# Kernel optimization log

Measured on AMD Instinct MI355X. Metric: run time of the kernel, lower is better.

The kernel has to match this reference:

```python
import jax, jax.numpy as jnp
import numpy as np

T_STEPS = 10       # T_pos = T_neg = 10 hardcoded in forward
ATTN_SCALE = 0.125 # scale hardcoded in forward (not head_dim**-0.5)
V_TH = 1.0         # spikingjelly IFNode defaults: v_threshold=1.0, v_reset=0.0 (hard reset)
SG_ALPHA = 4.0     # default Sigmoid surrogate alpha

@jax.custom_vjp
def spike(v):
    return (v >= 0.0).astype(v.dtype)

def _spike_fwd(v):
    return spike(v), v

def _spike_bwd(v, g):
    sg = jax.nn.sigmoid(SG_ALPHA * v)
    return (g * SG_ALPHA * sg * (1.0 - sg),)

spike.defvjp(_spike_fwd, _spike_bwd)

def if_node_const_input(y, T=T_STEPS):
    """Multi-step IF neuron driven by the SAME input y at every step.
    charge: v += y; fire: s = H(v - 1); hard reset: v = (1 - s) * v.
    Returns spikes of shape [T, *y.shape]."""
    def step(v, _):
        v = v + y
        s = spike(v - V_TH)
        v = (1.0 - s) * v
        return v, s
    _, spikes = jax.lax.scan(step, jnp.zeros_like(y), None, length=T)
    return spikes

def setup_inputs() -> dict:
    key = jax.random.key(0)
    ks = jax.random.split(key, 6)
    N, C = 2048, 2048
    x = jax.random.normal(ks[0], (N, C), dtype=jnp.float32)
    freqs_cis = jax.random.normal(ks[1], (N, 64), dtype=jnp.float32)  # unused by forward
    w_scale = 0.02
    wq = jax.random.normal(ks[2], (C, C), dtype=jnp.float32) * w_scale
    wk = jax.random.normal(ks[3], (C, C), dtype=jnp.float32) * w_scale
    wv = jax.random.normal(ks[4], (C, C), dtype=jnp.float32) * w_scale
    wo = jax.random.normal(ks[5], (C, C), dtype=jnp.float32) * w_scale
    return {"x": x, "freqs_cis": freqs_cis, "wq": wq, "wk": wk, "wv": wv, "wo": wo}

def reference(x, freqs_cis, wq, wk, wv, wo):
    N, C = x.shape
    n_heads, head_dim = 16, 128  # C == n_heads * head_dim; n_kv_heads == n_heads so repeat_kv is a no-op
    T = T_STEPS

    x_pos = jax.nn.relu(x)
    x_neg = jax.nn.relu(-x)

    # Input is identical at every timestep, so apply the linear once, then run IF over T.
    def branch(xb):
        q = if_node_const_input(xb @ wq)  # [T, N, C] binary spikes
        k = if_node_const_input(xb @ wk)
        v = if_node_const_input(xb @ wv)
        return q, k, v

    qp, kp, vp = branch(x_pos)
    qn, kn, vn = branch(x_neg)
    xq = (qp - qn).reshape(T, N, n_heads, head_dim)
    xk = (kp - kn).reshape(T, N, n_heads, head_dim)
    xv = (vp - vn).reshape(T, N, n_heads, head_dim)

    # no-softmax attention over the HEAD axis, per token: [T,N,H,H]
    attn = jnp.einsum('tnhd,tnmd->tnhm', xq, xk) * ATTN_SCALE
    x_attn = jnp.einsum('tnhm,tnmd->tnhd', attn, xv)          # [T,N,H,Dh]
    x_attn = jnp.swapaxes(x_attn, -1, -2).reshape(T, N, C)    # transpose(-1,-2) then merge

    xo = x_attn @ wo  # [T, N, C]
    return xo.mean(axis=0)
```

## Files before the change

### kernel.cpp

```cpp
#include <hip/hip_runtime.h>
#include <hip/hip_bf16.h>


#define LIST_CAP (512u * 1024u)
#define FLAG_EPS 4e-4f

typedef __attribute__((ext_vector_type(8))) short short8;
typedef __attribute__((ext_vector_type(4))) float floatx4;

__device__ const unsigned d_LUT[16] = {0u, 0x3FFu, 0x2AAu, 0x124u, 0x88u,
                                       0x210u, 0x20u, 0x40u, 0x80u, 0x100u,
                                       0x200u, 0u, 0u, 0u, 0u, 0u};

__device__ __forceinline__ void bf16x2_rne(float a, unsigned& p1, unsigned& p2) {
  const unsigned u = __float_as_uint(a);
  const unsigned t1 = u + 0x7FFFu + ((u >> 16) & 1u);
  p1 = t1 >> 16;
  const float r = a - __uint_as_float(t1 & 0xFFFF0000u);
  const unsigned u2 = __float_as_uint(r);
  p2 = (u2 + 0x7FFFu + ((u2 >> 16) & 1u)) >> 16;
}

template <int ZERO_CNT>
__global__ __launch_bounds__(256) void wsplit(
    const float* __restrict__ W0, const float* __restrict__ W1,
    const float* __restrict__ W2, unsigned short* __restrict__ Bpk,
    int NCT, unsigned* __restrict__ cnt) {
  if (ZERO_CNT && blockIdx.x == 0 && blockIdx.y == 0 && threadIdx.x == 0)
    *cnt = 0u;
  __shared__ float Wf[32 * 132];
  const int ct = blockIdx.x, k0 = blockIdx.y * 32;
  const int c0 = ct * 128;
  const int sel = c0 >> 11;
  const float* W = (sel == 0) ? W0 : ((sel == 1) ? W1 : W2);
  const int cc0 = c0 & 2047;
  const int t = threadIdx.x;

  const int kr = t >> 3, cq = (t & 7) * 16;
#pragma unroll
  for (int u = 0; u < 4; u++) {
    const float4 v = *(const float4*)(W + (size_t)(k0 + kr) * 2048 + cc0 + cq + 4 * u);
    *(float4*)&Wf[kr * 132 + cq + 4 * u] = v;
  }
  __syncthreads();

  const int cc = t >> 1, ch0 = (t & 1) * 2;
  unsigned short* img1 = Bpk + ((size_t)(0 * NCT + ct) * 64 + blockIdx.y) * 4096;
  unsigned short* img2 = Bpk + ((size_t)(1 * NCT + ct) * 64 + blockIdx.y) * 4096;
#pragma unroll
  for (int c = ch0; c < ch0 + 2; c++) {
    unsigned q1[8], q2[8];
#pragma unroll
    for (int e = 0; e < 8; e++) bf16x2_rne(Wf[(c * 8 + e) * 132 + cc], q1[e], q2[e]);
    const int off = cc * 32 + 8 * (c ^ ((cc >> 1) & 3));
    uint4 P1, P2;
    P1.x = q1[0] | (q1[1] << 16); P1.y = q1[2] | (q1[3] << 16);
    P1.z = q1[4] | (q1[5] << 16); P1.w = q1[6] | (q1[7] << 16);
    P2.x = q2[0] | (q2[1] << 16); P2.y = q2[2] | (q2[3] << 16);
    P2.z = q2[4] | (q2[5] << 16); P2.w = q2[6] | (q2[7] << 16);
    *(uint4*)&img1[off] = P1;
    *(uint4*)&img2[off] = P2;
  }
}

template <int RELU>
__global__ __launch_bounds__(256) void asplit(
    const float* __restrict__ src, unsigned short* __restrict__ Apk, int NRT) {
  const int rt = blockIdx.x, k0i = blockIdx.y;
  const int t = threadIdx.x;
  const int r = t >> 1, half = t & 1;
  int grow = rt * 128 + r;
  float sgn = 1.f;
  if (RELU && grow >= 2048) { grow -= 2048; sgn = -1.f; }
  const float* s = src + (size_t)grow * 2048 + k0i * 32 + half * 16;
  float f[16];
#pragma unroll
  for (int u = 0; u < 4; u++) {
    const float4 v = *(const float4*)(s + 4 * u);
    f[4 * u + 0] = v.x; f[4 * u + 1] = v.y;
    f[4 * u + 2] = v.z; f[4 * u + 3] = v.w;
  }
  if (RELU) {
#pragma unroll
    for (int e = 0; e < 16; e++) f[e] = fmaxf(sgn * f[e], 0.f);
  }
  unsigned q1[16], q2[16];
#pragma unroll
  for (int e = 0; e < 16; e++) bf16x2_rne(f[e], q1[e], q2[e]);

  unsigned short* img1 = Apk + ((size_t)(0 * NRT + rt) * 64 + k0i) * 4096;
  unsigned short* img2 = Apk + ((size_t)(1 * NRT + rt) * 64 + k0i) * 4096;
#pragma unroll
  for (int cc = 0; cc < 2; cc++) {
    const int c = half * 2 + cc;
    const int off = r * 32 + 8 * (c ^ ((r >> 1) & 3));
    const int e0 = cc * 8;
    uint4 P1, P2;
    P1.x = q1[e0 + 0] | (q1[e0 + 1] << 16); P1.y = q1[e0 + 2] | (q1[e0 + 3] << 16);
    P1.z = q1[e0 + 4] | (q1[e0 + 5] << 16); P1.w = q1[e0 + 6] | (q1[e0 + 7] << 16);
    P2.x = q2[e0 + 0] | (q2[e0 + 1] << 16); P2.y = q2[e0 + 2] | (q2[e0 + 3] << 16);
    P2.z = q2[e0 + 4] | (q2[e0 + 5] << 16); P2.w = q2[e0 + 6] | (q2[e0 + 7] << 16);
    *(uint4*)&img1[off] = P1;
    *(uint4*)&img2[off] = P2;
  }
}

template <int MODE>
__global__ __launch_bounds__(256) void gemm_dma(
    const unsigned short* __restrict__ Apk, const unsigned short* __restrict__ Bpk,
    int NRT, int NCT, unsigned char* __restrict__ MaskJ,
    unsigned* __restrict__ list, unsigned* __restrict__ cnt,
    float* __restrict__ Out) {
  __shared__ unsigned short sh[2][4][4096];
  __shared__ unsigned lutS[16];

  const int tid = threadIdx.x;
  const int bx = blockIdx.x, by = blockIdx.y;
  const int lane = tid & 63, wave = tid >> 6;
  const int wr = wave >> 1, wc = wave & 1;
  const int lm = lane & 15, lg = lane >> 4;

  if (MODE == 0 && tid < 16) lutS[tid] = d_LUT[tid];

  const unsigned short* gsrc =
      (wave < 2) ? (Apk + ((size_t)(wave * NRT + by) * 64) * 4096)
                 : (Bpk + ((size_t)((wave - 2) * NCT + bx) * 64) * 4096);

  auto dma8 = [&](unsigned short* dst, const unsigned short* src) {
#pragma unroll
    for (int i = 0; i < 8; i++) {
      __builtin_amdgcn_global_load_lds(
          (const __attribute__((address_space(1))) unsigned*)(src + i * 512 + lane * 8),
          (__attribute__((address_space(3))) unsigned*)(dst + i * 512), 16, 0, 0);
    }
  };

  floatx4 acc[4][4];
#pragma unroll
  for (int i = 0; i < 4; i++)
#pragma unroll
    for (int j = 0; j < 4; j++) acc[i][j] = (floatx4){0.f, 0.f, 0.f, 0.f};

  dma8(&sh[0][wave][0], gsrc);

  for (int k0i = 0; k0i < 64; k0i++) {
    __syncthreads();
    if (k0i + 1 < 64)
      dma8(&sh[(k0i + 1) & 1][wave][0], gsrc + (size_t)(k0i + 1) * 4096);

    const unsigned short(*cur)[4096] = sh[k0i & 1];
    short8 a1[4], a2[4], b1[4], b2[4];
#pragma unroll
    for (int i = 0; i < 4; i++) {
      const int row = 64 * wr + 16 * i + lm;
      const int off = row * 32 + 8 * (lg ^ ((row >> 1) & 3));
      a1[i] = *(const short8*)&cur[0][off];
      a2[i] = *(const short8*)&cur[1][off];
    }
#pragma unroll
    for (int j = 0; j < 4; j++) {
      const int row = 64 * wc + 16 * j + lm;
      const int off = row * 32 + 8 * (lg ^ ((row >> 1) & 3));
      b1[j] = *(const short8*)&cur[2][off];
      b2[j] = *(const short8*)&cur[3][off];
    }
#pragma unroll
    for (int i = 0; i < 4; i++)
#pragma unroll
      for (int j = 0; j < 4; j++)
        acc[i][j] = __builtin_amdgcn_mfma_f32_16x16x32_bf16(a1[i], b1[j], acc[i][j], 0, 0, 0);
#pragma unroll
    for (int i = 0; i < 4; i++)
#pragma unroll
      for (int j = 0; j < 4; j++)
        acc[i][j] = __builtin_amdgcn_mfma_f32_16x16x32_bf16(a1[i], b2[j], acc[i][j], 0, 0, 0);
#pragma unroll
    for (int i = 0; i < 4; i++)
#pragma unroll
      for (int j = 0; j < 4; j++)
        acc[i][j] = __builtin_amdgcn_mfma_f32_16x16x32_bf16(a2[i], b1[j], acc[i][j], 0, 0, 0);
  }

#pragma unroll
  for (int i = 0; i < 4; i++) {
#pragma unroll
    for (int j = 0; j < 4; j++) {
      const int gn = bx * 128 + 64 * wc + 16 * j + lm;
#pragma unroll
      for (int vv = 0; vv < 4; vv++) {
        const int gm = by * 128 + 64 * wr + 16 * i + 4 * lg + vv;
        const float y = acc[i][j][vv];
        if (MODE == 1) {
          Out[(size_t)gm * 2048 + gn] = y * 0.1f;
        } else {
          float r = __builtin_amdgcn_rcpf(y);
          r = fminf(fmaxf(r, -1.0f), 12.0f);
          const float jf = floorf(r);
          const float d0 = fmaf(jf, y, -1.0f);
          const float i0 = fminf(fmaxf(jf, 1.0f), 10.0f);
          const float i1 = fminf(fmaxf(jf + 1.0f, 1.0f), 10.0f);
          const float e0 = fmaf(i0, y, -1.0f);
          const float e1 = fmaf(i1, y, -1.0f);
          const float mind = fminf(fabsf(e0), fabsf(e1));
          const unsigned J = (unsigned)(int)((d0 >= 0.0f) ? jf : jf + 1.0f);
          MaskJ[(size_t)gm * 6144 + gn] = (unsigned char)((J <= 10u) ? J : 0u);
          if (mind < FLAG_EPS) {
            const unsigned idx = atomicAdd(cnt, 1u);
            if (idx < LIST_CAP) list[idx] = ((unsigned)gm << 13) | (unsigned)gn;
          }
        }
      }
    }
  }
}

__global__ __launch_bounds__(256) void transpose_w(
    const float* __restrict__ W0, const float* __restrict__ W1,
    const float* __restrict__ W2, float* __restrict__ WT) {
  __shared__ float tile[32][33];
  const int k0 = blockIdx.x * 32;
  const int c0 = blockIdx.y * 32;
  const int sel = c0 >> 11;
  const float* W = (sel == 0) ? W0 : ((sel == 1) ? W1 : W2);
  const int cc0 = c0 & 2047;
  const int tx = threadIdx.x, ty = threadIdx.y;
#pragma unroll
  for (int rep = 0; rep < 4; rep++)
    tile[ty + 8 * rep][tx] = W[(size_t)(k0 + ty + 8 * rep) * 2048 + cc0 + tx];
  __syncthreads();
#pragma unroll
  for (int rep = 0; rep < 4; rep++)
    WT[(size_t)(c0 + ty + 8 * rep) * 2048 + k0 + tx] = tile[tx][ty + 8 * rep];
}

__global__ __launch_bounds__(256) void rescue(
    const float* __restrict__ X, const float* __restrict__ WT,
    const unsigned* __restrict__ list, const unsigned* __restrict__ cnt,
    unsigned char* __restrict__ MaskJ) {
  const unsigned nItems = min(*cnt, LIST_CAP);
  const unsigned gtid = blockIdx.x * blockDim.x + threadIdx.x;
  const unsigned wave = gtid >> 6, lane = gtid & 63;
  const unsigned nWaves = (gridDim.x * blockDim.x) >> 6;

  for (unsigned i = wave; i < nItems; i += nWaves) {
    const unsigned e = list[i];
    const int r = (int)(e >> 13), c = (int)(e & 8191u);
    const float* xrow = X + (size_t)((r < 2048) ? r : r - 2048) * 2048;
    const float sg = (r < 2048) ? 1.f : -1.f;
    const float* wrow = WT + (size_t)c * 2048;
    double s = 0.0;
#pragma unroll
    for (int it = 0; it < 8; it++) {
      const int k = (it * 64 + (int)lane) * 4;
      const float4 xv = *(const float4*)(xrow + k);
      const float4 wv = *(const float4*)(wrow + k);
      const float a0 = fmaxf(sg * xv.x, 0.f);
      const float a1 = fmaxf(sg * xv.y, 0.f);
      const float a2 = fmaxf(sg * xv.z, 0.f);
      const float a3 = fmaxf(sg * xv.w, 0.f);
      s += (double)a0 * (double)wv.x + (double)a1 * (double)wv.y +
           (double)a2 * (double)wv.z + (double)a3 * (double)wv.w;
    }
#pragma unroll
    for (int off = 32; off > 0; off >>= 1) s += __shfl_down(s, off);
    if (lane == 0) {
      double v = 0.0;
      unsigned J = 0;
#pragma unroll
      for (int t = 0; t < 10; t++) {
        v += s;
        if (J == 0u && v >= 1.0) J = (unsigned)(t + 1);
      }
      MaskJ[(size_t)r * 6144 + c] = (unsigned char)J;
    }
  }
}

__global__ __launch_bounds__(256) void spike_attn(const unsigned char* __restrict__ MaskJ,
                                                  float* __restrict__ xbar) {
  const int n = blockIdx.x;
  const int tid = threadIdx.x;
  const int lane = tid & 63;

  __shared__ unsigned long long qpB[16][2], qnB[16][2], kpB[16][2], knB[16][2];
  __shared__ float xvT[16 * 132];
  __shared__ float attnS[16 * 17];
  __shared__ unsigned lutS[16];

  if (tid < 16) lutS[tid] = d_LUT[tid];
  __syncthreads();

  const unsigned char* mp = MaskJ + (size_t)n * 6144;
  const unsigned char* mn = MaskJ + (size_t)(n + 2048) * 6144;

  unsigned q_p[8], q_n[8], k_p[8], k_n[8], v_p[8], v_n[8];
#pragma unroll
  for (int j = 0; j < 8; j++) {
    const int c = tid + 256 * j;
    q_p[j] = lutS[mp[c]];        q_n[j] = lutS[mn[c]];
    k_p[j] = lutS[mp[2048 + c]]; k_n[j] = lutS[mn[2048 + c]];
    v_p[j] = lutS[mp[4096 + c]]; v_n[j] = lutS[mn[4096 + c]];
  }

  float acc[8];
#pragma unroll
  for (int j = 0; j < 8; j++) acc[j] = 0.f;

  for (int t = 0; t < 10; t++) {
#pragma unroll
    for (int j = 0; j < 8; j++) {
      const int c = tid + 256 * j;
      const unsigned long long bqp = __ballot((q_p[j] >> t) & 1u);
      const unsigned long long bqn = __ballot((q_n[j] >> t) & 1u);
      const unsigned long long bkp = __ballot((k_p[j] >> t) & 1u);
      const unsigned long long bkn = __ballot((k_n[j] >> t) & 1u);
      const int h = c >> 7, word = (c >> 6) & 1;
      if (lane == 0) {
        qpB[h][word] = bqp; qnB[h][word] = bqn;
        kpB[h][word] = bkp; knB[h][word] = bkn;
      }
      const int m = h, d = c & 127;
      xvT[m * 132 + d] =
          (float)((v_p[j] >> t) & 1u) - (float)((v_n[j] >> t) & 1u);
    }
    __syncthreads();

    {
      const int h = tid >> 4, m = tid & 15;
      int dot = 0;
#pragma unroll
      for (int w = 0; w < 2; w++) {
        const unsigned long long qp = qpB[h][w], qn = qnB[h][w];
        const unsigned long long kp = kpB[m][w], kn = knB[m][w];
        dot += __popcll(qp & kp) + __popcll(qn & kn) -
               __popcll(qp & kn) - __popcll(qn & kp);
      }
      attnS[h * 17 + m] = (float)dot * 0.125f;
    }
    __syncthreads();

    {
      const int h = tid & 15;
      float arow[16];
#pragma unroll
      for (int m = 0; m < 16; m++) arow[m] = attnS[h * 17 + m];
#pragma unroll
      for (int j = 0; j < 8; j++) {
        const int d = (tid + 256 * j) >> 4;
        float s = 0.f;
#pragma unroll
        for (int m = 0; m < 16; m++) s += arow[m] * xvT[m * 132 + d];
        acc[j] += s;
      }
    }
    __syncthreads();
  }

#pragma unroll
  for (int j = 0; j < 8; j++) xbar[(size_t)n * 2048 + tid + 256 * j] = acc[j];
}

extern "C" void kernel_launch(void* const* d_in, const int* in_sizes, int n_in,
                              void* d_out, int out_size, void* d_ws, size_t ws_size,
                              hipStream_t stream) {
  const float* x = (const float*)d_in[0];
  const float* wq = (const float*)d_in[2];
  const float* wk = (const float*)d_in[3];
  const float* wv = (const float*)d_in[4];
  const float* wo = (const float*)d_in[5];
  float* out = (float*)d_out;

  char* ws = (char*)d_ws;
  unsigned char* MaskJ = (unsigned char*)ws;
  unsigned short* WOpk = (unsigned short*)ws;
  char* reg2 = ws + (size_t)4096 * 6144;
  unsigned short* Bpk = (unsigned short*)reg2;
  float* WT = (float*)reg2;
  unsigned short* Xbpk = (unsigned short*)reg2;
  char* reg3 = reg2 + (size_t)6144 * 2048 * 2 * 2;
  unsigned short* Apk = (unsigned short*)reg3;
  float* xbar = (float*)reg3;
  unsigned* list = (unsigned*)(reg3 + (size_t)4096 * 2048 * 2 * 2);
  unsigned* cnt = list + LIST_CAP;

  wsplit<1><<<dim3(48, 64), 256, 0, stream>>>(wq, wk, wv, Bpk, 48, cnt);
  asplit<1><<<dim3(32, 64), 256, 0, stream>>>(x, Apk, 32);
  gemm_dma<0><<<dim3(48, 32), 256, 0, stream>>>(Apk, Bpk, 32, 48, MaskJ, list, cnt, nullptr);
  transpose_w<<<dim3(64, 192), dim3(32, 8), 0, stream>>>(wq, wk, wv, WT);
  rescue<<<2048, 256, 0, stream>>>(x, WT, list, cnt, MaskJ);
  spike_attn<<<2048, 256, 0, stream>>>(MaskJ, xbar);
  wsplit<0><<<dim3(16, 64), 256, 0, stream>>>(wo, wo, wo, WOpk, 16, nullptr);
  asplit<0><<<dim3(16, 64), 256, 0, stream>>>(xbar, Xbpk, 16);
  gemm_dma<1><<<dim3(16, 16), 256, 0, stream>>>(Xbpk, WOpk, 16, 16, nullptr, nullptr, nullptr, out);
}
```

Baseline: 838.6 us.

## Swizzle GEMM block order into 8x8 groups and drop LDS double buffering

Both GEMM launches switch to a 1D grid that is remapped into 8x8 supertiles of output blocks, so neighbouring blocks share A and B panels in L2. The LDS staging is cut from double-buffered to single-buffered: each k-step issues its DMA, waits on a barrier, then computes. This halves shared memory per block, which can raise occupancy, but it removes the overlap between global loads and MFMA work inside a block.

Result: no change. 847.8 us (+1.1%).

```diff
diff --git a/kernel.cpp b/kernel.cpp
--- a/kernel.cpp
+++ b/kernel.cpp
@@ -108,14 +108,18 @@
 template <int MODE>
 __global__ __launch_bounds__(256) void gemm_dma(
     const unsigned short* __restrict__ Apk, const unsigned short* __restrict__ Bpk,
-    int NRT, int NCT, unsigned char* __restrict__ MaskJ,
+    int NRT, int NCT, int SX, unsigned char* __restrict__ MaskJ,
     unsigned* __restrict__ list, unsigned* __restrict__ cnt,
     float* __restrict__ Out) {
-  __shared__ unsigned short sh[2][4][4096];
+  __shared__ unsigned short sh[4][4096];
   __shared__ unsigned lutS[16];
 
   const int tid = threadIdx.x;
-  const int bx = blockIdx.x, by = blockIdx.y;
+  const int id = blockIdx.x;
+  const int st = id >> 6, w = id & 63;
+  const int bx = (st % SX) * 8 + (w & 7);
+  const int by = (st / SX) * 8 + ((w >> 3) & 7);
+
   const int lane = tid & 63, wave = tid >> 6;
   const int wr = wave >> 1, wc = wave & 1;
   const int lm = lane & 15, lg = lane >> 4;
@@ -126,43 +130,37 @@
       (wave < 2) ? (Apk + ((size_t)(wave * NRT + by) * 64) * 4096)
                  : (Bpk + ((size_t)((wave - 2) * NCT + bx) * 64) * 4096);
 
-  auto dma8 = [&](unsigned short* dst, const unsigned short* src) {
+  floatx4 acc[4][4];
+#pragma unroll
+  for (int i = 0; i < 4; i++)
+#pragma unroll
+    for (int j = 0; j < 4; j++) acc[i][j] = (floatx4){0.f, 0.f, 0.f, 0.f};
+
+  for (int k0i = 0; k0i < 64; k0i++) {
+    __syncthreads();
+    const unsigned short* gp = gsrc + (size_t)k0i * 4096;
 #pragma unroll
     for (int i = 0; i < 8; i++) {
       __builtin_amdgcn_global_load_lds(
-          (const __attribute__((address_space(1))) unsigned*)(src + i * 512 + lane * 8),
-          (__attribute__((address_space(3))) unsigned*)(dst + i * 512), 16, 0, 0);
-    }
-  };
-
-  floatx4 acc[4][4];
-#pragma unroll
-  for (int i = 0; i < 4; i++)
-#pragma unroll
-    for (int j = 0; j < 4; j++) acc[i][j] = (floatx4){0.f, 0.f, 0.f, 0.f};
-
-  dma8(&sh[0][wave][0], gsrc);
-
-  for (int k0i = 0; k0i < 64; k0i++) {
-    __syncthreads();
-    if (k0i + 1 < 64)
-      dma8(&sh[(k0i + 1) & 1][wave][0], gsrc + (size_t)(k0i + 1) * 4096);
-
-    const unsigned short(*cur)[4096] = sh[k0i & 1];
+          (const __attribute__((address_space(1))) unsigned*)(gp + i * 512 + lane * 8),
+          (__attribute__((address_space(3))) unsigned*)(&sh[wave][i * 512]), 16, 0, 0);
+    }
+    __syncthreads();
+
     short8 a1[4], a2[4], b1[4], b2[4];
 #pragma unroll
     for (int i = 0; i < 4; i++) {
       const int row = 64 * wr + 16 * i + lm;
       const int off = row * 32 + 8 * (lg ^ ((row >> 1) & 3));
-      a1[i] = *(const short8*)&cur[0][off];
-      a2[i] = *(const short8*)&cur[1][off];
+      a1[i] = *(const short8*)&sh[0][off];
+      a2[i] = *(const short8*)&sh[1][off];
     }
 #pragma unroll
     for (int j = 0; j < 4; j++) {
       const int row = 64 * wc + 16 * j + lm;
       const int off = row * 32 + 8 * (lg ^ ((row >> 1) & 3));
-      b1[j] = *(const short8*)&cur[2][off];
-      b2[j] = *(const short8*)&cur[3][off];
+      b1[j] = *(const short8*)&sh[2][off];
+      b2[j] = *(const short8*)&sh[3][off];
     }
 #pragma unroll
     for (int i = 0; i < 4; i++)
@@ -385,11 +383,11 @@
 
   wsplit<1><<<dim3(48, 64), 256, 0, stream>>>(wq, wk, wv, Bpk, 48, cnt);
   asplit<1><<<dim3(32, 64), 256, 0, stream>>>(x, Apk, 32);
-  gemm_dma<0><<<dim3(48, 32), 256, 0, stream>>>(Apk, Bpk, 32, 48, MaskJ, list, cnt, nullptr);
+  gemm_dma<0><<<1536, 256, 0, stream>>>(Apk, Bpk, 32, 48, 6, MaskJ, list, cnt, nullptr);
   transpose_w<<<dim3(64, 192), dim3(32, 8), 0, stream>>>(wq, wk, wv, WT);
   rescue<<<2048, 256, 0, stream>>>(x, WT, list, cnt, MaskJ);
   spike_attn<<<2048, 256, 0, stream>>>(MaskJ, xbar);
   wsplit<0><<<dim3(16, 64), 256, 0, stream>>>(wo, wo, wo, WOpk, 16, nullptr);
   asplit<0><<<dim3(16, 64), 256, 0, stream>>>(xbar, Xbpk, 16);
-  gemm_dma<1><<<dim3(16, 16), 256, 0, stream>>>(Xbpk, WOpk, 16, 16, nullptr, nullptr, nullptr, out);
-}
+  gemm_dma<1><<<256, 256, 0, stream>>>(Xbpk, WOpk, 16, 16, 2, nullptr, nullptr, nullptr, out);
+}
```
